# Optimization experiments

Measured on AMD Instinct MI355X. Metric: run time of the kernel, lower is better.

Reference implementation:

```python
import jax, jax.numpy as jnp
import numpy as np

T = 2048          # tokens (prefill)
HID = 7168        # hidden_size
H = 16            # num_local_heads
NOPE = 128        # qk_nope_head_dim
ROPE = 64         # qk_rope_head_dim
VD = 128          # v_head_dim
QLR = 1536        # q_lora_rank
KVLR = 512        # kv_lora_rank
IH = 32           # index_n_heads
ID = 128          # index_head_dim
TOPK = 512        # index_topk
EPS = 1e-6
SCALE = float((NOPE + ROPE) ** -0.5)
ISCALE = float(ID ** -0.5)
ROPE_BASE = 10000.0


def setup_inputs() -> dict:
    key = jax.random.key(0)
    ks = jax.random.split(key, 10)
    def w(k, i, o):
        return jax.random.normal(k, (i, o), jnp.float32) * (i ** -0.5)
    return {
        'positions': jnp.arange(T, dtype=jnp.int32),
        'hidden': jax.random.normal(ks[0], (T, HID), jnp.float32),
        'q_c': jax.random.normal(ks[1], (T, QLR), jnp.float32),
        'kv_c': jax.random.normal(ks[2], (T, KVLR), jnp.float32),
        'k_pe': jax.random.normal(ks[3], (T, ROPE), jnp.float32),
        'q_a_ln_w': jnp.ones((QLR,), jnp.float32),
        'kv_a_ln_w': jnp.ones((KVLR,), jnp.float32),
        'Wq_b': w(ks[4], QLR, H * (NOPE + ROPE)),
        'Wkv_b': w(ks[5], KVLR, H * (NOPE + VD)),
        'Wo': w(ks[6], H * VD, HID),
        'Wiq': w(ks[7], QLR, IH * ID),
        'Wik': w(ks[8], HID, ID),
        'ik_gamma': jnp.ones((ID,), jnp.float32),
        'ik_beta': jnp.zeros((ID,), jnp.float32),
        'Ww': w(ks[9], HID, IH),
    }


def _rmsnorm(x, w):
    return x * jax.lax.rsqrt(jnp.mean(x * x, axis=-1, keepdims=True) + EPS) * w


def _layernorm(x, g, b):
    mu = jnp.mean(x, axis=-1, keepdims=True)
    var = jnp.mean((x - mu) ** 2, axis=-1, keepdims=True)
    return (x - mu) * jax.lax.rsqrt(var + EPS) * g + b


def _bc(c, x):
    # broadcast [T, d/2] cos/sin to x's rank ([T, d] or [T, H, d])
    return c.reshape(c.shape[0], *([1] * (x.ndim - 2)), c.shape[1])


def _rope_interleaved(x, cos, sin):
    # non-neox: pairs (x[2i], x[2i+1]) rotated (main MLA q_pe / k_pe)
    c, s = _bc(cos, x), _bc(sin, x)
    xe, xo = x[..., 0::2], x[..., 1::2]
    return jnp.stack([xe * c - xo * s, xo * c + xe * s], axis=-1).reshape(x.shape)


def _rope_neox(x, cos, sin):
    # neox: halves rotated (indexer rope, is_neox_style=True)
    c, s = _bc(cos, x), _bc(sin, x)
    x1, x2 = jnp.split(x, 2, axis=-1)
    return jnp.concatenate([x1 * c - x2 * s, x2 * c + x1 * s], axis=-1)


def reference(positions, hidden, q_c, kv_c, k_pe, q_a_ln_w, kv_a_ln_w,
              Wq_b, Wkv_b, Wo, Wiq, Wik, ik_gamma, ik_beta, Ww):
    t = hidden.shape[0]
    inv_freq = 1.0 / (ROPE_BASE ** (jnp.arange(0, ROPE, 2, dtype=jnp.float32) / ROPE))
    ang = positions.astype(jnp.float32)[:, None] * inv_freq        # [T, ROPE/2]
    cos, sin = jnp.cos(ang), jnp.sin(ang)

    # ---- low-rank Q / KV projections ----
    qc_n = _rmsnorm(q_c, q_a_ln_w)                                  # [T, QLR]
    q = (qc_n @ Wq_b).reshape(t, H, NOPE + ROPE)
    q_nope, q_pe = q[..., :NOPE], q[..., NOPE:]
    q_pe = _rope_interleaved(q_pe, cos, sin)                        # [T, H, ROPE]
    kv_n = _rmsnorm(kv_c, kv_a_ln_w)                                # [T, KVLR]
    kv = (kv_n @ Wkv_b).reshape(t, H, NOPE + VD)
    k_nope, v = kv[..., :NOPE], kv[..., NOPE:]
    k_pe_r = _rope_interleaved(k_pe, cos, sin)                      # [T, ROPE]

    # ---- lightning indexer: per-token relevance scores + top-k ----
    q_idx = (qc_n @ Wiq).reshape(t, IH, ID)
    q_idx = jnp.concatenate([_rope_neox(q_idx[..., :ROPE], cos, sin), q_idx[..., ROPE:]], axis=-1)
    k_idx = _layernorm(hidden @ Wik, ik_gamma, ik_beta)             # [T, ID]
    k_idx = jnp.concatenate([_rope_neox(k_idx[:, :ROPE], cos, sin), k_idx[:, ROPE:]], axis=-1)
    w_idx = (hidden @ Ww) * (IH ** -0.5)                            # [T, IH]
    logits = jnp.einsum('thd,jd->thj', q_idx, k_idx) * ISCALE       # [T, IH, T]
    scores = jnp.einsum('th,thj->tj', w_idx, jax.nn.relu(logits))   # [T, T]
    causal = jnp.tril(jnp.ones((t, t), bool))
    scores = jnp.where(causal, scores, -jnp.inf)
    _, topk_idx = jax.lax.top_k(scores, TOPK)                       # [T, TOPK]
    allowed = jnp.zeros((t, t), bool).at[jnp.arange(t)[:, None], topk_idx].set(True) & causal

    # ---- sparse MLA attention over selected tokens ----
    att = (jnp.einsum('thd,jhd->thj', q_nope, k_nope)
           + jnp.einsum('thd,jd->thj', q_pe, k_pe_r)) * SCALE       # [T, H, T]
    att = jnp.where(allowed[:, None, :], att, -jnp.inf)
    p = jax.nn.softmax(att, axis=-1)
    o = jnp.einsum('thj,jhd->thd', p, v).reshape(t, H * VD)
    return o @ Wo                                                    # [T, HID]
```

## Files before the change

kernel.cpp:

```cpp
#include <hip/hip_runtime.h>
#include <hip/hip_bf16.h>
#include <math.h>


namespace {

constexpr int T_    = 2048;
constexpr int HID_  = 7168;
constexpr int H_    = 16;
constexpr int QLR_  = 1536;
constexpr int KVLR_ = 512;
constexpr int IH_   = 32;
constexpr int ID_   = 128;
constexpr int TOPK_ = 512;
constexpr float EPS_    = 1e-6f;
constexpr float SCALE_  = 0.07216878364870322f;
constexpr float ISCALE_ = 0.08838834764831845f;
constexpr float WSCALE_ = 0.17677669529663687f;

constexpr int KSPLIT_ = 8;
constexpr int KC_     = HID_ / KSPLIT_;
constexpr int NC_     = 160;

typedef __attribute__((ext_vector_type(8))) short bf16x8;
typedef __attribute__((ext_vector_type(4))) float f32x4;

__device__ __forceinline__ unsigned int mono(float x) {
  unsigned int u = __float_as_uint(x);
  return (u & 0x80000000u) ? ~u : (u | 0x80000000u);
}

__device__ __forceinline__ unsigned short f2bf(float x) {
  unsigned int u = __float_as_uint(x);
  u += 0x7FFFu + ((u >> 16) & 1u);
  return (unsigned short)(u >> 16);
}

__device__ __forceinline__ float bf2f(unsigned short h) {
  return __uint_as_float((unsigned int)h << 16);
}

__global__ void k_tables(const int* __restrict__ pos, float* __restrict__ cosT,
                         float* __restrict__ sinT) {
  int idx = blockIdx.x * 256 + threadIdx.x;
  if (idx >= T_ * 32) return;
  int t = idx >> 5, i = idx & 31;
  float invf = (float)pow(10000.0, -(double)i / 32.0);
  float ang = (float)pos[t] * invf;
  cosT[idx] = cosf(ang);
  sinT[idx] = sinf(ang);
}

template <int N>
__launch_bounds__(256)
__global__ void k_rms(const float* __restrict__ x, const float* __restrict__ w,
                      unsigned short* __restrict__ yhi, unsigned short* __restrict__ ylo) {
  int t = blockIdx.x;
  const float* xr = x + (size_t)t * N;
  float ss = 0.f;
  for (int c = threadIdx.x; c < N; c += 256) { float v = xr[c]; ss += v * v; }
  __shared__ float red[256];
  red[threadIdx.x] = ss;
  __syncthreads();
  for (int off = 128; off > 0; off >>= 1) {
    if (threadIdx.x < off) red[threadIdx.x] += red[threadIdx.x + off];
    __syncthreads();
  }
  float sc = rsqrtf(red[0] * (1.f / N) + EPS_);
  unsigned short* yhr = yhi + (size_t)t * N;
  unsigned short* ylr = ylo ? ylo + (size_t)t * N : nullptr;
  for (int c = threadIdx.x; c < N; c += 256) {
    float v = xr[c] * sc * w[c];
    unsigned short hb = f2bf(v);
    yhr[c] = hb;
    if (ylr) ylr[c] = f2bf(v - bf2f(hb));
  }
}

__launch_bounds__(256)
__global__ void k_tc(const float* __restrict__ W, unsigned short* __restrict__ Wt,
                     int K, int N) {
  __shared__ float tile[64][65];
  int k0 = blockIdx.y * 64, n0 = blockIdx.x * 64;
  int tid = threadIdx.x;
#pragma unroll
  for (int i = 0; i < 16; ++i) {
    int e = i * 256 + tid;
    int r = e >> 6, c = e & 63;
    tile[r][c] = W[(size_t)(k0 + r) * N + n0 + c];
  }
  __syncthreads();
#pragma unroll
  for (int i = 0; i < 16; ++i) {
    int e = i * 256 + tid;
    int r = e >> 6, c = e & 63;
    Wt[(size_t)(n0 + r) * K + k0 + c] = f2bf(tile[c][r]);
  }
}

__launch_bounds__(256)
__global__ void k_tc2(const float* __restrict__ W, unsigned short* __restrict__ Wth,
                      unsigned short* __restrict__ Wtl, int K, int N) {
  __shared__ float tile[64][65];
  int k0 = blockIdx.y * 64, n0 = blockIdx.x * 64;
  int tid = threadIdx.x;
#pragma unroll
  for (int i = 0; i < 16; ++i) {
    int e = i * 256 + tid;
    int r = e >> 6, c = e & 63;
    tile[r][c] = W[(size_t)(k0 + r) * N + n0 + c];
  }
  __syncthreads();
#pragma unroll
  for (int i = 0; i < 16; ++i) {
    int e = i * 256 + tid;
    int r = e >> 6, c = e & 63;
    float v = tile[c][r];
    unsigned short hb = f2bf(v);
    size_t o = (size_t)(n0 + r) * K + k0 + c;
    Wth[o] = hb;
    Wtl[o] = f2bf(v - bf2f(hb));
  }
}

__launch_bounds__(256)
__global__ void k_tc2w(const float* __restrict__ Wik, const float* __restrict__ Ww,
                       unsigned short* __restrict__ Bth, unsigned short* __restrict__ Btl) {
  __shared__ float tile[64][65];
  int k0 = blockIdx.x * 64;
  int ny = blockIdx.y;
  int ncols = (ny == 2) ? 32 : 64;
  int tid = threadIdx.x;
#pragma unroll
  for (int i = 0; i < 16; ++i) {
    int e = i * 256 + tid;
    int r = e >> 6, c = e & 63;
    if (c < ncols)
      tile[r][c] = (ny == 2) ? Ww[(size_t)(k0 + r) * 32 + c]
                             : Wik[(size_t)(k0 + r) * 128 + ny * 64 + c];
  }
  __syncthreads();
#pragma unroll
  for (int i = 0; i < 16; ++i) {
    int e = i * 256 + tid;
    int r = e >> 6, c = e & 63;
    if (r < ncols) {
      float v = tile[c][r];
      unsigned short hb = f2bf(v);
      size_t o = (size_t)(ny * 64 + r) * HID_ + k0 + c;
      Bth[o] = hb;
      Btl[o] = f2bf(v - bf2f(hb));
    }
  }
}

__launch_bounds__(256)
__global__ void k_gemm_bf(const unsigned short* __restrict__ A,
                          const unsigned short* __restrict__ Bt,
                          float* __restrict__ C, int M, int N, int K) {
  __shared__ unsigned short As[128][40];
  __shared__ unsigned short Bs[128][40];
  int m0 = blockIdx.y * 128, n0 = blockIdx.x * 128;
  int tid = threadIdx.x;
  int w = tid >> 6, lane = tid & 63;
  int quad = lane >> 4, l16 = lane & 15;
  int wr = w & 1, wc = w >> 1;
  f32x4 acc[4][4] = {};
  for (int k0 = 0; k0 < K; k0 += 32) {
    __syncthreads();
#pragma unroll
    for (int i = 0; i < 2; ++i) {
      int c = i * 256 + tid;
      int row = c >> 2, off = (c & 3) * 8;
      *(uint4*)&As[row][off] = *(const uint4*)&A[(size_t)(m0 + row) * K + k0 + off];
      *(uint4*)&Bs[row][off] = *(const uint4*)&Bt[(size_t)(n0 + row) * K + k0 + off];
    }
    __syncthreads();
    bf16x8 a[4], b[4];
#pragma unroll
    for (int mi = 0; mi < 4; ++mi) a[mi] = *(const bf16x8*)&As[64 * wr + 16 * mi + l16][quad * 8];
#pragma unroll
    for (int ni = 0; ni < 4; ++ni) b[ni] = *(const bf16x8*)&Bs[64 * wc + 16 * ni + l16][quad * 8];
#pragma unroll
    for (int mi = 0; mi < 4; ++mi)
#pragma unroll
      for (int ni = 0; ni < 4; ++ni)
        acc[mi][ni] = __builtin_amdgcn_mfma_f32_16x16x32_bf16(a[mi], b[ni], acc[mi][ni], 0, 0, 0);
  }
#pragma unroll
  for (int mi = 0; mi < 4; ++mi)
#pragma unroll
    for (int ni = 0; ni < 4; ++ni)
#pragma unroll
      for (int r = 0; r < 4; ++r) {
        int row = m0 + 64 * wr + 16 * mi + quad * 4 + r;
        int col = n0 + 64 * wc + 16 * ni + l16;
        C[(size_t)row * N + col] = acc[mi][ni][r];
      }
}

__launch_bounds__(256)
__global__ void k_gemm3(const unsigned short* __restrict__ Ah,
                        const unsigned short* __restrict__ Al,
                        const unsigned short* __restrict__ Bth,
                        const unsigned short* __restrict__ Btl,
                        float* __restrict__ C, int M, int N, int K) {
  __shared__ unsigned short Ash[128][40];
  __shared__ unsigned short Asl[128][40];
  __shared__ unsigned short Bsh[128][40];
  __shared__ unsigned short Bsl[128][40];
  int m0 = blockIdx.y * 128, n0 = blockIdx.x * 128;
  int tid = threadIdx.x;
  int w = tid >> 6, lane = tid & 63;
  int quad = lane >> 4, l16 = lane & 15;
  int wr = w & 1, wc = w >> 1;
  f32x4 acc[4][4] = {};
  for (int k0 = 0; k0 < K; k0 += 32) {
    __syncthreads();
#pragma unroll
    for (int i = 0; i < 2; ++i) {
      int c = i * 256 + tid;
      int row = c >> 2, off = (c & 3) * 8;
      *(uint4*)&Ash[row][off] = *(const uint4*)&Ah[(size_t)(m0 + row) * K + k0 + off];
      *(uint4*)&Asl[row][off] = *(const uint4*)&Al[(size_t)(m0 + row) * K + k0 + off];
      *(uint4*)&Bsh[row][off] = *(const uint4*)&Bth[(size_t)(n0 + row) * K + k0 + off];
      *(uint4*)&Bsl[row][off] = *(const uint4*)&Btl[(size_t)(n0 + row) * K + k0 + off];
    }
    __syncthreads();
    bf16x8 ah[4], al[4];
#pragma unroll
    for (int mi = 0; mi < 4; ++mi) {
      ah[mi] = *(const bf16x8*)&Ash[64 * wr + 16 * mi + l16][quad * 8];
      al[mi] = *(const bf16x8*)&Asl[64 * wr + 16 * mi + l16][quad * 8];
    }
#pragma unroll
    for (int nh = 0; nh < 2; ++nh) {
      bf16x8 bh[2], bl[2];
#pragma unroll
      for (int nj = 0; nj < 2; ++nj) {
        int nrow = 64 * wc + 16 * (2 * nh + nj) + l16;
        bh[nj] = *(const bf16x8*)&Bsh[nrow][quad * 8];
        bl[nj] = *(const bf16x8*)&Bsl[nrow][quad * 8];
      }
#pragma unroll
      for (int mi = 0; mi < 4; ++mi)
#pragma unroll
        for (int nj = 0; nj < 2; ++nj) {
          int ni = 2 * nh + nj;
          acc[mi][ni] = __builtin_amdgcn_mfma_f32_16x16x32_bf16(ah[mi], bh[nj], acc[mi][ni], 0, 0, 0);
          acc[mi][ni] = __builtin_amdgcn_mfma_f32_16x16x32_bf16(ah[mi], bl[nj], acc[mi][ni], 0, 0, 0);
          acc[mi][ni] = __builtin_amdgcn_mfma_f32_16x16x32_bf16(al[mi], bh[nj], acc[mi][ni], 0, 0, 0);
        }
    }
  }
#pragma unroll
  for (int mi = 0; mi < 4; ++mi)
#pragma unroll
    for (int ni = 0; ni < 4; ++ni)
#pragma unroll
      for (int r = 0; r < 4; ++r) {
        int row = m0 + 64 * wr + 16 * mi + quad * 4 + r;
        int col = n0 + 64 * wc + 16 * ni + l16;
        C[(size_t)row * N + col] = acc[mi][ni][r];
      }
}

__launch_bounds__(256)
__global__ void k_hgemm(const float* __restrict__ hidden,
                        const unsigned short* __restrict__ Bth,
                        const unsigned short* __restrict__ Btl,
                        float* __restrict__ part) {
  __shared__ unsigned short Ash[64][40];
  __shared__ unsigned short Asl[64][40];
  __shared__ unsigned short Bsh[NC_][40];
  __shared__ unsigned short Bsl[NC_][40];
  int ks = blockIdx.x, m0 = blockIdx.y * 64;
  int kc0 = ks * KC_;
  int tid = threadIdx.x;
  int w = tid >> 6, lane = tid & 63;
  int quad = lane >> 4, l16 = lane & 15;
  int wr = w & 1, wc = w >> 1;
  f32x4 acc[2][5] = {};
  for (int s = 0; s < KC_ / 32; ++s) {
    int k0 = kc0 + s * 32;
    __syncthreads();
#pragma unroll
    for (int i = 0; i < 2; ++i) {
      int c = i * 256 + tid;
      int row = c >> 3, off = (c & 7) * 4;
      float4 v = *(const float4*)&hidden[(size_t)(m0 + row) * HID_ + k0 + off];
      ushort4 hv, lv;
      hv.x = f2bf(v.x); lv.x = f2bf(v.x - bf2f(hv.x));
      hv.y = f2bf(v.y); lv.y = f2bf(v.y - bf2f(hv.y));
      hv.z = f2bf(v.z); lv.z = f2bf(v.z - bf2f(hv.z));
      hv.w = f2bf(v.w); lv.w = f2bf(v.w - bf2f(hv.w));
      *(ushort4*)&Ash[row][off] = hv;
      *(ushort4*)&Asl[row][off] = lv;
    }
#pragma unroll
    for (int i = 0; i < 3; ++i) {
      int c = i * 256 + tid;
      if (c < NC_ * 4) {
        int row = c >> 2, off = (c & 3) * 8;
        *(uint4*)&Bsh[row][off] = *(const uint4*)&Bth[(size_t)row * HID_ + k0 + off];
        *(uint4*)&Bsl[row][off] = *(const uint4*)&Btl[(size_t)row * HID_ + k0 + off];
      }
    }
    __syncthreads();
    bf16x8 ah[2], al[2];
#pragma unroll
    for (int mi = 0; mi < 2; ++mi) {
      ah[mi] = *(const bf16x8*)&Ash[32 * wr + 16 * mi + l16][quad * 8];
      al[mi] = *(const bf16x8*)&Asl[32 * wr + 16 * mi + l16][quad * 8];
    }
#pragma unroll
    for (int ni = 0; ni < 5; ++ni) {
      int nrow = 80 * wc + 16 * ni + l16;
      bf16x8 bh = *(const bf16x8*)&Bsh[nrow][quad * 8];
      bf16x8 bl = *(const bf16x8*)&Bsl[nrow][quad * 8];
#pragma unroll
      for (int mi = 0; mi < 2; ++mi) {
        acc[mi][ni] = __builtin_amdgcn_mfma_f32_16x16x32_bf16(ah[mi], bh, acc[mi][ni], 0, 0, 0);
        acc[mi][ni] = __builtin_amdgcn_mfma_f32_16x16x32_bf16(ah[mi], bl, acc[mi][ni], 0, 0, 0);
        acc[mi][ni] = __builtin_amdgcn_mfma_f32_16x16x32_bf16(al[mi], bh, acc[mi][ni], 0, 0, 0);
      }
    }
  }
#pragma unroll
  for (int mi = 0; mi < 2; ++mi)
#pragma unroll
    for (int ni = 0; ni < 5; ++ni)
#pragma unroll
      for (int r = 0; r < 4; ++r) {
        int row = m0 + 32 * wr + 16 * mi + quad * 4 + r;
        int col = 80 * wc + 16 * ni + l16;
        part[((size_t)ks * T_ + row) * NC_ + col] = acc[mi][ni][r];
      }
}

__launch_bounds__(192)
__global__ void k_kidx_fin(const float* __restrict__ part,
                           const float* __restrict__ gamma, const float* __restrict__ beta,
                           const float* __restrict__ cosT, const float* __restrict__ sinT,
                           unsigned short* __restrict__ kh, unsigned short* __restrict__ kl,
                           float* __restrict__ widx) {
  int t = blockIdx.x;
  int tid = threadIdx.x;
  float y = 0.f;
  if (tid < NC_) {
#pragma unroll
    for (int s = 0; s < KSPLIT_; ++s) y += part[((size_t)s * T_ + t) * NC_ + tid];
  }
  __shared__ float red[128];
  __shared__ float sm2[2];
  __shared__ float yn[128];
  if (tid < 128) red[tid] = y;
  __syncthreads();
  for (int off = 64; off > 0; off >>= 1) {
    if (tid < off) red[tid] += red[tid + off];
    __syncthreads();
  }
  if (tid == 0) sm2[0] = red[0] * (1.f / 128.f);
  __syncthreads();
  float mu = sm2[0];
  if (tid < 128) { float d = y - mu; red[tid] = d * d; }
  __syncthreads();
  for (int off = 64; off > 0; off >>= 1) {
    if (tid < off) red[tid] += red[tid + off];
    __syncthreads();
  }
  if (tid == 0) sm2[1] = red[0] * (1.f / 128.f);
  __syncthreads();
  if (tid < 128) {
    float rstd = rsqrtf(sm2[1] + EPS_);
    yn[tid] = (y - mu) * rstd * gamma[tid] + beta[tid];
  }
  __syncthreads();
  if (tid < 32) {
    int i = tid;
    float co = cosT[t * 32 + i], si = sinT[t * 32 + i];
    float a = yn[i], b = yn[i + 32];
    float v0 = a * co - b * si;
    float v1 = b * co + a * si;
    unsigned short h0 = f2bf(v0);
    kh[(size_t)t * ID_ + i] = h0;
    kl[(size_t)t * ID_ + i] = f2bf(v0 - bf2f(h0));
    unsigned short h1 = f2bf(v1);
    kh[(size_t)t * ID_ + i + 32] = h1;
    kl[(size_t)t * ID_ + i + 32] = f2bf(v1 - bf2f(h1));
  } else if (tid >= 64 && tid < 128) {
    float v = yn[tid];
    unsigned short hb = f2bf(v);
    kh[(size_t)t * ID_ + tid] = hb;
    kl[(size_t)t * ID_ + tid] = f2bf(v - bf2f(hb));
  } else if (tid >= 128 && tid < 160) {
    widx[(size_t)t * 32 + (tid - 128)] = y * WSCALE_;
  }
}

__global__ void k_rope_q(float* __restrict__ q, const float* __restrict__ cosT,
                         const float* __restrict__ sinT) {
  int idx = blockIdx.x * 256 + threadIdx.x;
  if (idx >= T_ * H_ * 32) return;
  int i = idx & 31;
  int th = idx >> 5;
  int h = th & 15, t = th >> 4;
  float c = cosT[t * 32 + i], s = sinT[t * 32 + i];
  float* p = q + (size_t)t * 3072 + h * 192 + 128 + 2 * i;
  float e = p[0], o = p[1];
  p[0] = e * c - o * s;
  p[1] = o * c + e * s;
}

__launch_bounds__(256)
__global__ void k_qidx_prep(const float* __restrict__ qidx,
                            const float* __restrict__ cosT, const float* __restrict__ sinT,
                            unsigned short* __restrict__ qh, unsigned short* __restrict__ ql) {
  int t = blockIdx.x;
  int tid = threadIdx.x;
#pragma unroll
  for (int m = 0; m < 4; ++m) {
    int e = m * 256 + tid;
    int h = e >> 5, i = e & 31;
    float c = cosT[t * 32 + i], s = sinT[t * 32 + i];
    const float* p = qidx + (size_t)t * 4096 + h * 128;
    float a = p[i], b = p[i + 32];
    float o0 = a * c - b * s;
    float o1 = b * c + a * s;
    size_t base = ((size_t)h * T_ + t) * 128;
    unsigned short h0 = f2bf(o0);
    qh[base + i] = h0;
    ql[base + i] = f2bf(o0 - bf2f(h0));
    unsigned short h1 = f2bf(o1);
    qh[base + i + 32] = h1;
    ql[base + i + 32] = f2bf(o1 - bf2f(h1));
  }
#pragma unroll
  for (int m = 0; m < 8; ++m) {
    int e = m * 256 + tid;
    int h = e >> 6, d = 64 + (e & 63);
    float v = qidx[(size_t)t * 4096 + h * 128 + d];
    size_t o = ((size_t)h * T_ + t) * 128 + d;
    unsigned short hb = f2bf(v);
    qh[o] = hb;
    ql[o] = f2bf(v - bf2f(hb));
  }
}

__global__ void k_rope_kpe(const float* __restrict__ kpe, const float* __restrict__ cosT,
                           const float* __restrict__ sinT, float* __restrict__ kper) {
  int idx = blockIdx.x * 256 + threadIdx.x;
  if (idx >= T_ * 32) return;
  int i = idx & 31, t = idx >> 5;
  float c = cosT[idx], s = sinT[idx];
  float e = kpe[(size_t)t * 64 + 2 * i], o = kpe[(size_t)t * 64 + 2 * i + 1];
  kper[(size_t)t * 64 + 2 * i] = e * c - o * s;
  kper[(size_t)t * 64 + 2 * i + 1] = o * c + e * s;
}

__launch_bounds__(256)
__global__ void k_scores_mfma(const unsigned short* __restrict__ qh,
                              const unsigned short* __restrict__ ql,
                              const unsigned short* __restrict__ kh,
                              const unsigned short* __restrict__ kl,
                              const float* __restrict__ widx,
                              float* __restrict__ scores) {
  int jb = blockIdx.x, tb = blockIdx.y;
  int t0 = tb * 32, j0 = jb * 64;
  if (j0 > t0 + 31) return;
  __shared__ unsigned short Ksh[64][136];
  __shared__ unsigned short Ksl[64][136];
  __shared__ unsigned short Qsh[32][136];
  __shared__ unsigned short Qsl[32][136];
  __shared__ float Wsh[32][33];
  int tid = threadIdx.x;
#pragma unroll
  for (int i = 0; i < 4; ++i) {
    int e = i * 256 + tid;
    int r = e >> 4, off = (e & 15) * 8;
    *(uint4*)&Ksh[r][off] = *(const uint4*)&kh[(size_t)(j0 + r) * 128 + off];
    *(uint4*)&Ksl[r][off] = *(const uint4*)&kl[(size_t)(j0 + r) * 128 + off];
  }
#pragma unroll
  for (int i = 0; i < 4; ++i) {
    int e = i * 256 + tid;
    int r = e >> 5, c = e & 31;
    Wsh[r][c] = widx[(size_t)(t0 + r) * 32 + c];
  }
  int w = tid >> 6, lane = tid & 63;
  int quad = lane >> 4, l16 = lane & 15;
  int wr = w & 1, wc = w >> 1;
  float s0[4] = {0.f, 0.f, 0.f, 0.f};
  float s1[4] = {0.f, 0.f, 0.f, 0.f};
  for (int h = 0; h < 32; ++h) {
    __syncthreads();
#pragma unroll
    for (int i = 0; i < 2; ++i) {
      int e = i * 256 + tid;
      int r = e >> 4, off = (e & 15) * 8;
      size_t base = ((size_t)h * T_ + t0 + r) * 128 + off;
      *(uint4*)&Qsh[r][off] = *(const uint4*)&qh[base];
      *(uint4*)&Qsl[r][off] = *(const uint4*)&ql[base];
    }
    __syncthreads();
    f32x4 l0 = {}, l1 = {};
#pragma unroll
    for (int kk = 0; kk < 4; ++kk) {
      bf16x8 ah = *(const bf16x8*)&Qsh[16 * wr + l16][kk * 32 + quad * 8];
      bf16x8 al = *(const bf16x8*)&Qsl[16 * wr + l16][kk * 32 + quad * 8];
      bf16x8 bh0 = *(const bf16x8*)&Ksh[32 * wc + l16][kk * 32 + quad * 8];
      bf16x8 bl0 = *(const bf16x8*)&Ksl[32 * wc + l16][kk * 32 + quad * 8];
      bf16x8 bh1 = *(const bf16x8*)&Ksh[32 * wc + 16 + l16][kk * 32 + quad * 8];
      bf16x8 bl1 = *(const bf16x8*)&Ksl[32 * wc + 16 + l16][kk * 32 + quad * 8];
      l0 = __builtin_amdgcn_mfma_f32_16x16x32_bf16(ah, bh0, l0, 0, 0, 0);
      l0 = __builtin_amdgcn_mfma_f32_16x16x32_bf16(ah, bl0, l0, 0, 0, 0);
      l0 = __builtin_amdgcn_mfma_f32_16x16x32_bf16(al, bh0, l0, 0, 0, 0);
      l1 = __builtin_amdgcn_mfma_f32_16x16x32_bf16(ah, bh1, l1, 0, 0, 0);
      l1 = __builtin_amdgcn_mfma_f32_16x16x32_bf16(ah, bl1, l1, 0, 0, 0);
      l1 = __builtin_amdgcn_mfma_f32_16x16x32_bf16(al, bh1, l1, 0, 0, 0);
    }
#pragma unroll
    for (int r = 0; r < 4; ++r) {
      float wv = Wsh[16 * wr + quad * 4 + r][h];
      s0[r] = fmaf(wv, fmaxf(l0[r] * ISCALE_, 0.f), s0[r]);
      s1[r] = fmaf(wv, fmaxf(l1[r] * ISCALE_, 0.f), s1[r]);
    }
  }
#pragma unroll
  for (int r = 0; r < 4; ++r) {
    int row = t0 + 16 * wr + quad * 4 + r;
    scores[(size_t)row * T_ + j0 + 32 * wc + l16] = s0[r];
    scores[(size_t)row * T_ + j0 + 32 * wc + 16 + l16] = s1[r];
  }
}

__launch_bounds__(256)
__global__ void k_topk(const float* __restrict__ scores, unsigned int* __restrict__ kth) {
  int t = blockIdx.x;
  int n = t + 1;
  if (n <= TOPK_) {
    if (threadIdx.x == 0) kth[t] = 0u;
    return;
  }
  unsigned int keys[8];
#pragma unroll
  for (int m = 0; m < 8; ++m) {
    int j = threadIdx.x + m * 256;
    keys[m] = (j < n) ? mono(scores[(size_t)t * T_ + j]) : 0u;
  }
  __shared__ int wred[4];
  unsigned int thr = 0u;
  for (int b = 31; b >= 0; --b) {
    unsigned int cand = thr | (1u << b);
    int c = 0;
#pragma unroll
    for (int m = 0; m < 8; ++m) c += (keys[m] >= cand) ? 1 : 0;
    for (int o = 32; o > 0; o >>= 1) c += __shfl_down(c, o, 64);
    if ((threadIdx.x & 63) == 0) wred[threadIdx.x >> 6] = c;
    __syncthreads();
    int total = wred[0] + wred[1] + wred[2] + wred[3];
    if (total >= TOPK_) thr = cand;
    __syncthreads();
  }
  if (threadIdx.x == 0) kth[t] = thr;
}

__launch_bounds__(256)
__global__ void k_cast_flash(const float* __restrict__ qbuf, const float* __restrict__ kvb,
                             const float* __restrict__ kper,
                             unsigned short* __restrict__ Qb, unsigned short* __restrict__ Kb) {
  int t = blockIdx.x;
  int tid = threadIdx.x;
#pragma unroll
  for (int i = 0; i < 12; ++i) {
    int e = i * 256 + tid;
    int h = e / 192, d = e % 192;
    Qb[((size_t)h * T_ + t) * 192 + d] = f2bf(qbuf[(size_t)t * 3072 + e]);
    float kv = (d < 128) ? kvb[(size_t)t * 4096 + h * 256 + d]
                         : kper[(size_t)t * 64 + (d - 128)];
    Kb[((size_t)h * T_ + t) * 192 + d] = f2bf(kv);
  }
}

__launch_bounds__(256)
__global__ void k_cast_v(const float* __restrict__ kvb, unsigned short* __restrict__ Vt) {
  __shared__ unsigned short vt[128][137];
  int h = blockIdx.y, t0 = blockIdx.x * 128;
  int tid = threadIdx.x;
#pragma unroll
  for (int i = 0; i < 64; ++i) {
    int e = i * 256 + tid;
    int tl = e >> 7, d = e & 127;
    vt[tl][d] = f2bf(kvb[(size_t)(t0 + tl) * 4096 + h * 256 + 128 + d]);
  }
  __syncthreads();
#pragma unroll
  for (int i = 0; i < 64; ++i) {
    int e = i * 256 + tid;
    int d = e >> 7, tl = e & 127;
    Vt[((size_t)h * 128 + d) * T_ + t0 + tl] = vt[tl][d];
  }
}

__launch_bounds__(256)
__global__ void k_flash2(const unsigned short* __restrict__ Qb,
                         const unsigned short* __restrict__ Kb,
                         const unsigned short* __restrict__ Vt,
                         const float* __restrict__ scores,
                         const unsigned int* __restrict__ kth,
                         unsigned short* __restrict__ obf) {
  __shared__ unsigned short Qs[32][200];
  __shared__ unsigned short Ks[32][200];
  __shared__ unsigned short VsT[128][40];
  __shared__ float Ss[32][33];
  __shared__ unsigned short Ps[32][40];
  __shared__ float m_s[32], l_s[32], al_s[32];

  int t0 = blockIdx.x * 32, h = blockIdx.y;
  int tid = threadIdx.x;
  int w = tid >> 6, lane = tid & 63;
  int quad = lane >> 4, l16 = lane & 15;
  int wr = w & 1, wc = w >> 1;

#pragma unroll
  for (int i = 0; i < 3; ++i) {
    int c = i * 256 + tid;
    int row = c / 24, off = (c % 24) * 8;
    *(uint4*)&Qs[row][off] =
        *(const uint4*)&Qb[((size_t)h * T_ + t0 + row) * 192 + off];
  }
  if (tid < 32) { m_s[tid] = -INFINITY; l_s[tid] = 0.f; }

  f32x4 Of[4] = {};

  int srow = tid >> 3;
  int c8 = tid & 7;
  int ig = t0 + srow;

  int njt = blockIdx.x + 1;
  for (int jt = 0; jt < njt; ++jt) {
    int j0 = jt * 32;
    __syncthreads();
#pragma unroll
    for (int i = 0; i < 3; ++i) {
      int c = i * 256 + tid;
      int row = c / 24, off = (c % 24) * 8;
      *(uint4*)&Ks[row][off] =
          *(const uint4*)&Kb[((size_t)h * T_ + j0 + row) * 192 + off];
    }
#pragma unroll
    for (int i = 0; i < 2; ++i) {
      int c = i * 256 + tid;
      int d = c >> 2, off = (c & 3) * 8;
      *(uint4*)&VsT[d][off] =
          *(const uint4*)&Vt[((size_t)h * 128 + d) * T_ + j0 + off];
    }
    __syncthreads();

    f32x4 Sacc = {};
#pragma unroll
    for (int kk = 0; kk < 6; ++kk) {
      bf16x8 a = *(const bf16x8*)&Qs[16 * wr + l16][kk * 32 + quad * 8];
      bf16x8 b = *(const bf16x8*)&Ks[16 * wc + l16][kk * 32 + quad * 8];
      Sacc = __builtin_amdgcn_mfma_f32_16x16x32_bf16(a, b, Sacc, 0, 0, 0);
    }
#pragma unroll
    for (int r = 0; r < 4; ++r)
      Ss[16 * wr + quad * 4 + r][16 * wc + l16] = Sacc[r];
    __syncthreads();

    float mold = m_s[srow];
    unsigned int kt = kth[ig];
    float4 s4 = *(const float4*)(scores + (size_t)ig * T_ + j0 + 4 * c8);
    float sv[4] = {s4.x, s4.y, s4.z, s4.w};
    float v[4];
#pragma unroll
    for (int c = 0; c < 4; ++c) {
      int jg = j0 + 4 * c8 + c;
      float sc = Ss[srow][4 * c8 + c];
      bool ok = (jg <= ig) && (mono(sv[c]) >= kt);
      v[c] = ok ? sc * SCALE_ : -INFINITY;
    }
    float tmax = fmaxf(fmaxf(v[0], v[1]), fmaxf(v[2], v[3]));
#pragma unroll
    for (int o = 1; o < 8; o <<= 1) tmax = fmaxf(tmax, __shfl_xor(tmax, o, 8));
    float mn = fmaxf(mold, tmax);
    float alpha = (mold == -INFINITY) ? 0.f : expf(mold - mn);
    float p[4], psum = 0.f;
#pragma unroll
    for (int c = 0; c < 4; ++c) {
      p[c] = (v[c] == -INFINITY) ? 0.f : expf(v[c] - mn);
      psum += p[c];
    }
#pragma unroll
    for (int o = 1; o < 8; o <<= 1) psum += __shfl_xor(psum, o, 8);
    if (c8 == 0) {
      m_s[srow] = mn;
      al_s[srow] = alpha;
      l_s[srow] = alpha * l_s[srow] + psum;
    }
#pragma unroll
    for (int c = 0; c < 4; ++c) Ps[srow][4 * c8 + c] = f2bf(p[c]);
    __syncthreads();

    float arow[4];
#pragma unroll
    for (int r = 0; r < 4; ++r) arow[r] = al_s[16 * wr + quad * 4 + r];
    bf16x8 pa = *(const bf16x8*)&Ps[16 * wr + l16][quad * 8];
#pragma unroll
    for (int i = 0; i < 4; ++i) {
#pragma unroll
      for (int r = 0; r < 4; ++r) Of[i][r] *= arow[r];
      bf16x8 vb = *(const bf16x8*)&VsT[16 * (4 * wc + i) + l16][quad * 8];
      Of[i] = __builtin_amdgcn_mfma_f32_16x16x32_bf16(pa, vb, Of[i], 0, 0, 0);
    }
  }

  float linv[4];
#pragma unroll
  for (int r = 0; r < 4; ++r) linv[r] = 1.f / l_s[16 * wr + quad * 4 + r];
#pragma unroll
  for (int i = 0; i < 4; ++i) {
#pragma unroll
    for (int r = 0; r < 4; ++r) {
      int row = t0 + 16 * wr + quad * 4 + r;
      int col = 16 * (4 * wc + i) + l16;
      obf[(size_t)row * 2048 + h * 128 + col] = f2bf(Of[i][r] * linv[r]);
    }
  }
}

}

extern "C" void kernel_launch(void* const* d_in, const int* in_sizes, int n_in,
                              void* d_out, int out_size, void* d_ws, size_t ws_size,
                              hipStream_t stream) {
  (void)in_sizes; (void)n_in; (void)out_size; (void)ws_size;
  const int*   positions = (const int*)d_in[0];
  const float* hidden  = (const float*)d_in[1];
  const float* q_c     = (const float*)d_in[2];
  const float* kv_c    = (const float*)d_in[3];
  const float* k_pe    = (const float*)d_in[4];
  const float* q_ln    = (const float*)d_in[5];
  const float* kv_ln   = (const float*)d_in[6];
  const float* Wq_b    = (const float*)d_in[7];
  const float* Wkv_b   = (const float*)d_in[8];
  const float* Wo      = (const float*)d_in[9];
  const float* Wiq     = (const float*)d_in[10];
  const float* Wik     = (const float*)d_in[11];
  const float* ik_g    = (const float*)d_in[12];
  const float* ik_b    = (const float*)d_in[13];
  const float* Ww      = (const float*)d_in[14];
  float* out = (float*)d_out;

  float* ws = (float*)d_ws;
  size_t off = 0;
  float* cosT = ws + off; off += (size_t)T_ * 32;
  float* sinT = ws + off; off += (size_t)T_ * 32;
  float* qcn  = ws + off; off += (size_t)T_ * QLR_;
  float* kvn  = ws + off; off += (size_t)T_ * KVLR_;
  float* qbuf = ws + off; off += (size_t)T_ * H_ * 192;
  float* kvb  = ws + off; off += (size_t)T_ * H_ * 256;
  float* qidx = ws + off; off += (size_t)T_ * 4096;
  float* kidx = ws + off; off += (size_t)T_ * ID_;
  float* widx = ws + off; off += (size_t)T_ * IH_;
  float* kper = ws + off; off += (size_t)T_ * 64;
  float* scores = ws + off; off += (size_t)T_ * T_;
  unsigned int* kth = (unsigned int*)(ws + off); off += T_;
  unsigned short* qcn_bf = (unsigned short*)(ws + off); off += (size_t)T_ * QLR_ / 2;
  unsigned short* kvn_bf = (unsigned short*)(ws + off); off += (size_t)T_ * KVLR_ / 2;
  unsigned short* Wot = (unsigned short*)(ws + off); off += (size_t)HID_ * 2048 / 2;
  unsigned short* Vt  = (unsigned short*)(ws + off); off += (size_t)H_ * 128 * T_ / 2;
  unsigned short* qidx_h = (unsigned short*)(ws + off); off += (size_t)T_ * 4096 / 2;
  unsigned short* qidx_l = (unsigned short*)(ws + off); off += (size_t)T_ * 4096 / 2;
  unsigned short* Bikw_h = (unsigned short*)(ws + off); off += (size_t)NC_ * HID_ / 2;
  unsigned short* Bikw_l = (unsigned short*)(ws + off); off += (size_t)NC_ * HID_ / 2;
  (void)kidx;

  unsigned short* Wqt  = (unsigned short*)scores;
  unsigned short* Wkvt = Wqt + (size_t)3072 * 1536;
  float* hpart = scores;
  unsigned short* Qb   = (unsigned short*)qidx;
  unsigned short* Kb   = Qb + (size_t)H_ * T_ * 192;
  unsigned short* obf  = Kb + (size_t)H_ * T_ * 192;
  unsigned short* qcn_lo = (unsigned short*)qcn;
  unsigned short* kidx_h = (unsigned short*)kvn;
  unsigned short* kidx_l = kidx_h + (size_t)T_ * ID_;
  unsigned short* Wiqt_h = (unsigned short*)qbuf;
  unsigned short* Wiqt_l = Wiqt_h + (size_t)4096 * QLR_;

  k_tables<<<dim3(T_ * 32 / 256), dim3(256), 0, stream>>>(positions, cosT, sinT);
  k_rms<QLR_><<<dim3(T_), dim3(256), 0, stream>>>(q_c, q_ln, qcn_bf, qcn_lo);
  k_rms<KVLR_><<<dim3(T_), dim3(256), 0, stream>>>(kv_c, kv_ln, kvn_bf, nullptr);
  k_tc2<<<dim3(4096 / 64, QLR_ / 64), dim3(256), 0, stream>>>(Wiq, Wiqt_h, Wiqt_l, QLR_, 4096);
  k_gemm3<<<dim3(4096 / 128, T_ / 128), dim3(256), 0, stream>>>(qcn_bf, qcn_lo, Wiqt_h, Wiqt_l,
                                                                qidx, T_, 4096, QLR_);
  k_qidx_prep<<<dim3(T_), dim3(256), 0, stream>>>(qidx, cosT, sinT, qidx_h, qidx_l);
  k_tc<<<dim3(3072 / 64, QLR_ / 64), dim3(256), 0, stream>>>(Wq_b, Wqt, QLR_, 3072);
  k_tc<<<dim3(4096 / 64, KVLR_ / 64), dim3(256), 0, stream>>>(Wkv_b, Wkvt, KVLR_, 4096);
  k_tc<<<dim3(HID_ / 64, 2048 / 64), dim3(256), 0, stream>>>(Wo, Wot, 2048, HID_);
  k_tc2w<<<dim3(HID_ / 64, 3), dim3(256), 0, stream>>>(Wik, Ww, Bikw_h, Bikw_l);
  k_gemm_bf<<<dim3(3072 / 128, T_ / 128), dim3(256), 0, stream>>>(qcn_bf, Wqt, qbuf, T_, 3072, QLR_);
  k_rope_q<<<dim3(T_ * H_ * 32 / 256), dim3(256), 0, stream>>>(qbuf, cosT, sinT);
  k_gemm_bf<<<dim3(4096 / 128, T_ / 128), dim3(256), 0, stream>>>(kvn_bf, Wkvt, kvb, T_, 4096, KVLR_);
  k_hgemm<<<dim3(KSPLIT_, T_ / 64), dim3(256), 0, stream>>>(hidden, Bikw_h, Bikw_l, hpart);
  k_kidx_fin<<<dim3(T_), dim3(192), 0, stream>>>(hpart, ik_g, ik_b, cosT, sinT,
                                                 kidx_h, kidx_l, widx);
  k_rope_kpe<<<dim3(T_ * 32 / 256), dim3(256), 0, stream>>>(k_pe, cosT, sinT, kper);
  k_scores_mfma<<<dim3(T_ / 64, T_ / 32), dim3(256), 0, stream>>>(qidx_h, qidx_l, kidx_h, kidx_l,
                                                                  widx, scores);
  k_topk<<<dim3(T_), dim3(256), 0, stream>>>(scores, kth);
  k_cast_flash<<<dim3(T_), dim3(256), 0, stream>>>(qbuf, kvb, kper, Qb, Kb);
  k_cast_v<<<dim3(T_ / 128, H_), dim3(256), 0, stream>>>(kvb, Vt);
  k_flash2<<<dim3(T_ / 32, H_), dim3(256), 0, stream>>>(Qb, Kb, Vt, scores, kth, obf);
  k_gemm_bf<<<dim3(HID_ / 128, T_ / 128), dim3(256), 0, stream>>>(obf, Wot, out, T_, HID_, 2048);
}
```

Baseline: 961.1 us.

## Rewrite flash attention as per-wave 16-row tiles with causal load balancing

The flash kernel is restructured so each wave owns its own 16 query rows and keeps the online-softmax state in registers. Q, K and V are read straight from global memory, with no shared-memory staging and no block-wide barriers. Waves are paired with mirrored row indices (early plus late rows) so every block does a similar amount of causal work, and the grid shrinks to 32x16 blocks. The cost is that K and V are no longer shared across waves in LDS, so global/L2 traffic rises, and the grid is much smaller, which may lower occupancy.

```diff
diff --git a/kernel.cpp b/kernel.cpp
--- a/kernel.cpp
+++ b/kernel.cpp
@@ -603,131 +603,96 @@
 }
 
 __launch_bounds__(256)
-__global__ void k_flash2(const unsigned short* __restrict__ Qb,
+__global__ void k_flash3(const unsigned short* __restrict__ Qb,
                          const unsigned short* __restrict__ Kb,
                          const unsigned short* __restrict__ Vt,
                          const float* __restrict__ scores,
                          const unsigned int* __restrict__ kth,
                          unsigned short* __restrict__ obf) {
-  __shared__ unsigned short Qs[32][200];
-  __shared__ unsigned short Ks[32][200];
-  __shared__ unsigned short VsT[128][40];
-  __shared__ float Ss[32][33];
-  __shared__ unsigned short Ps[32][40];
-  __shared__ float m_s[32], l_s[32], al_s[32];
-
-  int t0 = blockIdx.x * 32, h = blockIdx.y;
-  int tid = threadIdx.x;
-  int w = tid >> 6, lane = tid & 63;
+  __shared__ unsigned short Ps[4][16][40];
+  int h = blockIdx.y;
+  int b = blockIdx.x;
+  int w = threadIdx.x >> 6, lane = threadIdx.x & 63;
   int quad = lane >> 4, l16 = lane & 15;
-  int wr = w & 1, wc = w >> 1;
-
-#pragma unroll
-  for (int i = 0; i < 3; ++i) {
-    int c = i * 256 + tid;
-    int row = c / 24, off = (c % 24) * 8;
-    *(uint4*)&Qs[row][off] =
-        *(const uint4*)&Qb[((size_t)h * T_ + t0 + row) * 192 + off];
-  }
-  if (tid < 32) { m_s[tid] = -INFINITY; l_s[tid] = 0.f; }
-
-  f32x4 Of[4] = {};
-
-  int srow = tid >> 3;
-  int c8 = tid & 7;
-  int ig = t0 + srow;
-
-  int njt = blockIdx.x + 1;
+  int r = (w < 2) ? (2 * b + w) : ((w == 2) ? (126 - 2 * b) : (127 - 2 * b));
+  int tq = r * 16;
+
+  bf16x8 aq[6];
+#pragma unroll
+  for (int kk = 0; kk < 6; ++kk)
+    aq[kk] = *(const bf16x8*)&Qb[((size_t)h * T_ + tq + l16) * 192 + kk * 32 + quad * 8];
+
+  unsigned int kt[4];
+  float m[4], l[4];
+#pragma unroll
+  for (int rr = 0; rr < 4; ++rr) {
+    kt[rr] = kth[tq + quad * 4 + rr];
+    m[rr] = -INFINITY;
+    l[rr] = 0.f;
+  }
+  f32x4 Of[8] = {};
+
+  int njt = (tq + 47) >> 5;
   for (int jt = 0; jt < njt; ++jt) {
     int j0 = jt * 32;
-    __syncthreads();
-#pragma unroll
-    for (int i = 0; i < 3; ++i) {
-      int c = i * 256 + tid;
-      int row = c / 24, off = (c % 24) * 8;
-      *(uint4*)&Ks[row][off] =
-          *(const uint4*)&Kb[((size_t)h * T_ + j0 + row) * 192 + off];
-    }
-#pragma unroll
-    for (int i = 0; i < 2; ++i) {
-      int c = i * 256 + tid;
-      int d = c >> 2, off = (c & 3) * 8;
-      *(uint4*)&VsT[d][off] =
-          *(const uint4*)&Vt[((size_t)h * 128 + d) * T_ + j0 + off];
-    }
-    __syncthreads();
-
-    f32x4 Sacc = {};
+    f32x4 S0 = {}, S1 = {};
 #pragma unroll
     for (int kk = 0; kk < 6; ++kk) {
-      bf16x8 a = *(const bf16x8*)&Qs[16 * wr + l16][kk * 32 + quad * 8];
-      bf16x8 b = *(const bf16x8*)&Ks[16 * wc + l16][kk * 32 + quad * 8];
-      Sacc = __builtin_amdgcn_mfma_f32_16x16x32_bf16(a, b, Sacc, 0, 0, 0);
-    }
-#pragma unroll
-    for (int r = 0; r < 4; ++r)
-      Ss[16 * wr + quad * 4 + r][16 * wc + l16] = Sacc[r];
-    __syncthreads();
-
-    float mold = m_s[srow];
-    unsigned int kt = kth[ig];
-    float4 s4 = *(const float4*)(scores + (size_t)ig * T_ + j0 + 4 * c8);
-    float sv[4] = {s4.x, s4.y, s4.z, s4.w};
-    float v[4];
-#pragma unroll
-    for (int c = 0; c < 4; ++c) {
-      int jg = j0 + 4 * c8 + c;
-      float sc = Ss[srow][4 * c8 + c];
-      bool ok = (jg <= ig) && (mono(sv[c]) >= kt);
-      v[c] = ok ? sc * SCALE_ : -INFINITY;
-    }
-    float tmax = fmaxf(fmaxf(v[0], v[1]), fmaxf(v[2], v[3]));
-#pragma unroll
-    for (int o = 1; o < 8; o <<= 1) tmax = fmaxf(tmax, __shfl_xor(tmax, o, 8));
-    float mn = fmaxf(mold, tmax);
-    float alpha = (mold == -INFINITY) ? 0.f : expf(mold - mn);
-    float p[4], psum = 0.f;
-#pragma unroll
-    for (int c = 0; c < 4; ++c) {
-      p[c] = (v[c] == -INFINITY) ? 0.f : expf(v[c] - mn);
-      psum += p[c];
-    }
-#pragma unroll
-    for (int o = 1; o < 8; o <<= 1) psum += __shfl_xor(psum, o, 8);
-    if (c8 == 0) {
-      m_s[srow] = mn;
-      al_s[srow] = alpha;
-      l_s[srow] = alpha * l_s[srow] + psum;
-    }
-#pragma unroll
-    for (int c = 0; c < 4; ++c) Ps[srow][4 * c8 + c] = f2bf(p[c]);
-    __syncthreads();
-
-    float arow[4];
-#pragma unroll
-    for (int r = 0; r < 4; ++r) arow[r] = al_s[16 * wr + quad * 4 + r];
-    bf16x8 pa = *(const bf16x8*)&Ps[16 * wr + l16][quad * 8];
-#pragma unroll
-    for (int i = 0; i < 4; ++i) {
-#pragma unroll
-      for (int r = 0; r < 4; ++r) Of[i][r] *= arow[r];
-      bf16x8 vb = *(const bf16x8*)&VsT[16 * (4 * wc + i) + l16][quad * 8];
-      Of[i] = __builtin_amdgcn_mfma_f32_16x16x32_bf16(pa, vb, Of[i], 0, 0, 0);
+      bf16x8 b0 = *(const bf16x8*)&Kb[((size_t)h * T_ + j0 + l16) * 192 + kk * 32 + quad * 8];
+      bf16x8 b1 = *(const bf16x8*)&Kb[((size_t)h * T_ + j0 + 16 + l16) * 192 + kk * 32 + quad * 8];
+      S0 = __builtin_amdgcn_mfma_f32_16x16x32_bf16(aq[kk], b0, S0, 0, 0, 0);
+      S1 = __builtin_amdgcn_mfma_f32_16x16x32_bf16(aq[kk], b1, S1, 0, 0, 0);
+    }
+    float al[4];
+#pragma unroll
+    for (int rr = 0; rr < 4; ++rr) {
+      int ig = tq + quad * 4 + rr;
+      int jg0 = j0 + l16, jg1 = j0 + 16 + l16;
+      float sv0 = scores[(size_t)ig * T_ + jg0];
+      float sv1 = scores[(size_t)ig * T_ + jg1];
+      bool ok0 = (jg0 <= ig) && (mono(sv0) >= kt[rr]);
+      bool ok1 = (jg1 <= ig) && (mono(sv1) >= kt[rr]);
+      float v0 = ok0 ? S0[rr] * SCALE_ : -INFINITY;
+      float v1 = ok1 ? S1[rr] * SCALE_ : -INFINITY;
+      float tm = fmaxf(v0, v1);
+#pragma unroll
+      for (int o = 1; o < 16; o <<= 1) tm = fmaxf(tm, __shfl_xor(tm, o, 16));
+      float mn = fmaxf(m[rr], tm);
+      al[rr] = (m[rr] == -INFINITY) ? 0.f : expf(m[rr] - mn);
+      float p0 = (v0 == -INFINITY) ? 0.f : expf(v0 - mn);
+      float p1 = (v1 == -INFINITY) ? 0.f : expf(v1 - mn);
+      float ps = p0 + p1;
+#pragma unroll
+      for (int o = 1; o < 16; o <<= 1) ps += __shfl_xor(ps, o, 16);
+      l[rr] = al[rr] * l[rr] + ps;
+      m[rr] = mn;
+      Ps[w][quad * 4 + rr][l16] = f2bf(p0);
+      Ps[w][quad * 4 + rr][16 + l16] = f2bf(p1);
+    }
+#pragma unroll
+    for (int db = 0; db < 8; ++db)
+#pragma unroll
+      for (int rr = 0; rr < 4; ++rr) Of[db][rr] *= al[rr];
+    asm volatile("s_waitcnt lgkmcnt(0)" ::: "memory");
+    __builtin_amdgcn_sched_barrier(0);
+    bf16x8 pa = *(const bf16x8*)&Ps[w][l16][quad * 8];
+#pragma unroll
+    for (int db = 0; db < 8; ++db) {
+      bf16x8 bv = *(const bf16x8*)&Vt[((size_t)h * 128 + db * 16 + l16) * T_ + j0 + quad * 8];
+      Of[db] = __builtin_amdgcn_mfma_f32_16x16x32_bf16(pa, bv, Of[db], 0, 0, 0);
     }
   }
 
   float linv[4];
 #pragma unroll
-  for (int r = 0; r < 4; ++r) linv[r] = 1.f / l_s[16 * wr + quad * 4 + r];
-#pragma unroll
-  for (int i = 0; i < 4; ++i) {
-#pragma unroll
-    for (int r = 0; r < 4; ++r) {
-      int row = t0 + 16 * wr + quad * 4 + r;
-      int col = 16 * (4 * wc + i) + l16;
-      obf[(size_t)row * 2048 + h * 128 + col] = f2bf(Of[i][r] * linv[r]);
-    }
-  }
+  for (int rr = 0; rr < 4; ++rr) linv[rr] = 1.f / l[rr];
+#pragma unroll
+  for (int db = 0; db < 8; ++db)
+#pragma unroll
+    for (int rr = 0; rr < 4; ++rr) {
+      int row = tq + quad * 4 + rr;
+      obf[(size_t)row * 2048 + h * 128 + db * 16 + l16] = f2bf(Of[db][rr] * linv[rr]);
+    }
 }
 
 }
@@ -812,6 +777,6 @@
   k_topk<<<dim3(T_), dim3(256), 0, stream>>>(scores, kth);
   k_cast_flash<<<dim3(T_), dim3(256), 0, stream>>>(qbuf, kvb, kper, Qb, Kb);
   k_cast_v<<<dim3(T_ / 128, H_), dim3(256), 0, stream>>>(kvb, Vt);
-  k_flash2<<<dim3(T_ / 32, H_), dim3(256), 0, stream>>>(Qb, Kb, Vt, scores, kth, obf);
+  k_flash3<<<dim3(32, H_), dim3(256), 0, stream>>>(Qb, Kb, Vt, scores, kth, obf);
   k_gemm_bf<<<dim3(HID_ / 128, T_ / 128), dim3(256), 0, stream>>>(obf, Wot, out, T_, HID_, 2048);
 }
```

Measured after the change: 1.030 ms. 1.07x slower.
